# Kernel tuning notes

Hardware: AMD Instinct MI355X
Metric: run time of the kernel (lower is better)

## Reference

```python
import jax, jax.numpy as jnp
import numpy as np

CUTOFF = 5.0
N_PER_L = (20, 18, 16, 14)   # radial features per angular channel l (max_radial=20, Laplacian-eigenstate style taper)
M_PER_L = (1, 3, 5, 7)       # 2l+1
N_ATOMS = 10000
N_EDGES = 200000
N_SPECIES = 100
PSEUDO = 4

_FREQS = np.concatenate([np.arange(1, nl + 1) for nl in N_PER_L]).astype(np.float32)  # [sum(N_PER_L)]


def _radial(r):
    # r: [P] -> [P, sum(N_PER_L)]. Sine (spherical Laplacian eigenstate style) basis with smooth cosine cutoff.
    rc = jnp.clip(r, 0.0, CUTOFF)
    fc = 0.5 * (jnp.cos(jnp.pi * rc / CUTOFF) + 1.0)            # [P]
    return jnp.sin(jnp.asarray(_FREQS) * (jnp.pi / CUTOFF) * r[:, None]) * fc[:, None]


def _angular(R, r):
    # real spherical harmonics up to l=3, [P, 16], ordered l-major (m = -l..l)
    u = R / (r[:, None] + 1e-12)
    x, y, z = u[:, 0], u[:, 1], u[:, 2]
    x2, y2, z2 = x * x, y * y, z * z
    cols = [
        jnp.full_like(x, 0.28209479177387814),
        0.4886025119029199 * y, 0.4886025119029199 * z, 0.4886025119029199 * x,
        1.0925484305920792 * x * y, 1.0925484305920792 * y * z,
        0.31539156525252005 * (3.0 * z2 - 1.0),
        1.0925484305920792 * x * z, 0.5462742152960396 * (x2 - y2),
        0.5900435899266435 * y * (3.0 * x2 - y2), 2.890611442640554 * x * y * z,
        0.4570457994644658 * y * (5.0 * z2 - 1.0), 0.3731763325901154 * z * (5.0 * z2 - 3.0),
        0.4570457994644658 * x * (5.0 * z2 - 1.0), 1.445305721320277 * z * (x2 - y2),
        0.5900435899266435 * x * (x2 - 3.0 * y2),
    ]
    return jnp.stack(cols, axis=-1)


def setup_inputs() -> dict:
    key = jax.random.key(0)
    k1, k2, k3, k4, k5 = jax.random.split(key, 5)
    return {
        "R_ij": jax.random.normal(k1, (N_EDGES, 3), dtype=jnp.float32) * 1.5,
        "i": jnp.sort(jax.random.randint(k2, (N_EDGES,), 0, N_ATOMS)),
        "j": jax.random.randint(k3, (N_EDGES,), 0, N_ATOMS),
        "species": jax.random.randint(k4, (N_ATOMS,), 0, N_SPECIES),
        "species_embed": jax.random.normal(k5, (N_SPECIES, PSEUDO), dtype=jnp.float32),
    }


def reference(R_ij, i, j, species, species_embed):
    r = jnp.sqrt(jnp.sum(R_ij * R_ij, axis=-1))          # [P]
    radial = _radial(r)                                   # [P, sum n_l]
    angular = _angular(R_ij, r)                           # [P, 16]
    sp = species_embed[species[j]]                        # alchemical species channels, [P, 4]
    outs = []
    off_n = 0
    off_m = 0
    for nl, ml in zip(N_PER_L, M_PER_L):
        rl = radial[:, off_n:off_n + nl]                  # [P, n_l]
        al = angular[:, off_m:off_m + ml]                 # [P, 2l+1]
        e = jnp.einsum('pn,pm,pc->pmnc', rl, al, sp)      # fused outer product per edge
        outs.append(jax.ops.segment_sum(e, i, num_segments=N_ATOMS))  # [n_atoms, 2l+1, n_l, 4]
        off_n += nl
        off_m += ml
    return tuple(outs)
```

## Files before the change

kernel.cpp:

```cpp
#include <hip/hip_runtime.h>

#define N_ATOMS 10000
#define N_EDGES 200000
#define EB 64
#define FEAT 40
#define PI_F 3.14159265358979323846f
#define W_F  0.6283185307179586f

__global__ __launch_bounds__(256) void seg_starts_kernel(
    const int* __restrict__ seg_i, int* __restrict__ starts)
{
    const int a = blockIdx.x * blockDim.x + threadIdx.x;
    if (a > N_ATOMS) return;
    int lo = 0, hi = N_EDGES;
    while (lo < hi) {
        int mid = (lo + hi) >> 1;
        if (seg_i[mid] < a) lo = mid + 1; else hi = mid;
    }
    starts[a] = lo;
}

__global__ __launch_bounds__(128) void sph_expand_kernel(
    const float* __restrict__ R,
    const int*   __restrict__ starts,
    const int*   __restrict__ idx_j,
    const int*   __restrict__ species,
    const float* __restrict__ emb,
    float*       __restrict__ out)
{
    __shared__ float feat[EB][FEAT];
    const int atom = blockIdx.x;
    const int tid  = threadIdx.x;

    int m, np_, nl, offm; long base; int stride;
    {
        int t = tid;
        if (t < 10)      { m = 0;                 np_ = t;          nl = 20; offm = 0; base = 0;        stride = 80;  }
        else if (t < 37) { int q = t - 10; m = q / 9; np_ = q - 9*m; nl = 18; offm = 1; base = 800000;  stride = 216; }
        else if (t < 77) { int q = t - 37; m = q / 8; np_ = q - 8*m; nl = 16; offm = 4; base = 2960000; stride = 320; }
        else             { int q = t - 77; m = q / 7; np_ = q - 7*m; nl = 14; offm = 9; base = 6160000; stride = 392; }
    }
    const int n0   = 2 * np_;
    const int aidx = 20 + offm + m;
    const bool active = (tid < 126);

    float a0x=0.f, a0y=0.f, a0z=0.f, a0w=0.f;
    float a1x=0.f, a1y=0.f, a1z=0.f, a1w=0.f;

    const int start = starts[atom];
    const int end   = starts[atom + 1];

    for (int e0 = start; e0 < end; e0 += EB) {
        const int cnt = min(EB, end - e0);
        __syncthreads();
        if (tid < cnt) {
            const int g = e0 + tid;
            const int jj = idx_j[g];
            const float x = R[3*g + 0];
            const float y = R[3*g + 1];
            const float z = R[3*g + 2];
            const int sidx = species[jj];
            const float r   = sqrtf(x*x + y*y + z*z);
            const float inv = 1.0f / (r + 1e-12f);
            const float ux = x*inv, uy = y*inv, uz = z*inv;
            const float4 spv = *(const float4*)&emb[4 * sidx];

            const float t1 = W_F * r;
            const float s1 = sinf(t1);
            const float c1 = cosf(t1);
            const float fc = (r < 5.0f) ? (0.5f * (c1 + 1.0f)) : 0.0f;
            const float c2x = 2.0f * c1;

            float rb[20];
            {
                float sk_2 = 0.0f, sk_1 = s1;
                rb[0] = s1 * fc;
                #pragma unroll
                for (int k = 1; k < 20; ++k) {
                    const float sk = c2x * sk_1 - sk_2;
                    rb[k] = sk * fc;
                    sk_2 = sk_1; sk_1 = sk;
                }
            }

            const float x2 = ux*ux, y2 = uy*uy, z2 = uz*uz;
            const float c1a = 0.4886025119029199f;
            const float c2a = 1.0925484305920792f;
            float an[16];
            an[0]  = 0.28209479177387814f;
            an[1]  = c1a * uy;
            an[2]  = c1a * uz;
            an[3]  = c1a * ux;
            an[4]  = c2a * ux * uy;
            an[5]  = c2a * uy * uz;
            an[6]  = 0.31539156525252005f * (3.0f*z2 - 1.0f);
            an[7]  = c2a * ux * uz;
            an[8]  = 0.5462742152960396f * (x2 - y2);
            an[9]  = 0.5900435899266435f * uy * (3.0f*x2 - y2);
            an[10] = 2.890611442640554f  * ux * uy * uz;
            an[11] = 0.4570457994644658f * uy * (5.0f*z2 - 1.0f);
            an[12] = 0.3731763325901154f * uz * (5.0f*z2 - 3.0f);
            an[13] = 0.4570457994644658f * ux * (5.0f*z2 - 1.0f);
            an[14] = 1.445305721320277f  * uz * (x2 - y2);
            an[15] = 0.5900435899266435f * ux * (x2 - 3.0f*y2);

            float4* row = (float4*)&feat[tid][0];
            row[0] = float4{rb[0],  rb[1],  rb[2],  rb[3]};
            row[1] = float4{rb[4],  rb[5],  rb[6],  rb[7]};
            row[2] = float4{rb[8],  rb[9],  rb[10], rb[11]};
            row[3] = float4{rb[12], rb[13], rb[14], rb[15]};
            row[4] = float4{rb[16], rb[17], rb[18], rb[19]};
            row[5] = float4{an[0],  an[1],  an[2],  an[3]};
            row[6] = float4{an[4],  an[5],  an[6],  an[7]};
            row[7] = float4{an[8],  an[9],  an[10], an[11]};
            row[8] = float4{an[12], an[13], an[14], an[15]};
            row[9] = spv;
        }
        __syncthreads();
        if (active) {
            for (int s = 0; s < cnt; ++s) {
                const float* f = &feat[s][0];
                const float2 rv  = *(const float2*)(f + n0);
                const float  av  = f[aidx];
                const float4 spv = *(const float4*)(f + 36);
                const float p0 = rv.x * av;
                const float p1 = rv.y * av;
                a0x += p0 * spv.x; a0y += p0 * spv.y; a0z += p0 * spv.z; a0w += p0 * spv.w;
                a1x += p1 * spv.x; a1y += p1 * spv.y; a1z += p1 * spv.z; a1w += p1 * spv.w;
            }
        }
    }

    if (active) {
        const size_t o = (size_t)base + (size_t)atom * (size_t)stride + (size_t)(m * nl + n0) * 4;
        *(float4*)&out[o]     = float4{a0x, a0y, a0z, a0w};
        *(float4*)&out[o + 4] = float4{a1x, a1y, a1z, a1w};
    }
}

extern "C" void kernel_launch(void* const* d_in, const int* in_sizes, int n_in,
                              void* d_out, int out_size, void* d_ws, size_t ws_size,
                              hipStream_t stream) {
    const float* R    = (const float*)d_in[0];
    const int*   i_   = (const int*)  d_in[1];
    const int*   j_   = (const int*)  d_in[2];
    const int*   sp   = (const int*)  d_in[3];
    const float* emb  = (const float*)d_in[4];
    float* out = (float*)d_out;
    int*   starts = (int*)d_ws;

    seg_starts_kernel<<<(N_ATOMS + 256) / 256, 256, 0, stream>>>(i_, starts);
    sph_expand_kernel<<<N_ATOMS, 128, 0, stream>>>(R, starts, j_, sp, emb, out);
}
```

Before: 92.31 us.

## Register-block 4 radial x 2 angular outputs per thread, shrink block to one wavefront

```diff
diff --git a/kernel.cpp b/kernel.cpp
--- a/kernel.cpp
+++ b/kernel.cpp
@@ -2,8 +2,8 @@
 
 #define N_ATOMS 10000
 #define N_EDGES 200000
-#define EB 64
-#define FEAT 40
+#define EB   32
+#define ROWF 44
 #define PI_F 3.14159265358979323846f
 #define W_F  0.6283185307179586f
 
@@ -20,7 +20,35 @@
     starts[a] = lo;
 }
 
-__global__ __launch_bounds__(128) void sph_expand_kernel(
+#define TE(n0,aidx,w,m1,nl4,str,off) \
+  {(unsigned)((n0)|((aidx)<<5)|((w)<<11)|((m1)<<14)|((nl4)<<15)|((unsigned)(str)<<22)), (unsigned)(off)}
+__device__ const uint2 TBL[43] = {
+    TE( 0,20,4,0,80, 80,      0), TE( 4,20,4,0,80, 80,     16),
+    TE( 8,20,4,0,80, 80,     32), TE(12,20,4,0,80, 80,     48),
+    TE(16,20,4,0,80, 80,     64),
+    TE( 0,22,4,1,72,216, 800000), TE( 4,22,4,1,72,216, 800016),
+    TE( 8,22,4,1,72,216, 800032), TE(12,22,4,1,72,216, 800048),
+    TE(16,22,2,1,72,216, 800064),
+    TE( 0,24,4,0,72,216, 800144), TE( 4,24,4,0,72,216, 800160),
+    TE( 8,24,4,0,72,216, 800176), TE(12,24,4,0,72,216, 800192),
+    TE(16,24,2,0,72,216, 800208),
+    TE( 0,26,4,1,64,320,2960000), TE( 4,26,4,1,64,320,2960016),
+    TE( 8,26,4,1,64,320,2960032), TE(12,26,4,1,64,320,2960048),
+    TE( 0,28,4,1,64,320,2960128), TE( 4,28,4,1,64,320,2960144),
+    TE( 8,28,4,1,64,320,2960160), TE(12,28,4,1,64,320,2960176),
+    TE( 0,30,4,0,64,320,2960256), TE( 4,30,4,0,64,320,2960272),
+    TE( 8,30,4,0,64,320,2960288), TE(12,30,4,0,64,320,2960304),
+    TE( 0,32,4,1,56,392,6160000), TE( 4,32,4,1,56,392,6160016),
+    TE( 8,32,4,1,56,392,6160032), TE(12,32,2,1,56,392,6160048),
+    TE( 0,34,4,1,56,392,6160112), TE( 4,34,4,1,56,392,6160128),
+    TE( 8,34,4,1,56,392,6160144), TE(12,34,2,1,56,392,6160160),
+    TE( 0,36,4,1,56,392,6160224), TE( 4,36,4,1,56,392,6160240),
+    TE( 8,36,4,1,56,392,6160256), TE(12,36,2,1,56,392,6160272),
+    TE( 0,38,4,0,56,392,6160336), TE( 4,38,4,0,56,392,6160352),
+    TE( 8,38,4,0,56,392,6160368), TE(12,38,2,0,56,392,6160384),
+};
+
+__global__ __launch_bounds__(64) void sph_expand_kernel(
     const float* __restrict__ R,
     const int*   __restrict__ starts,
     const int*   __restrict__ idx_j,
@@ -28,24 +56,21 @@
     const float* __restrict__ emb,
     float*       __restrict__ out)
 {
-    __shared__ float feat[EB][FEAT];
+    __shared__ float feat[EB * ROWF];
     const int atom = blockIdx.x;
     const int tid  = threadIdx.x;
 
-    int m, np_, nl, offm; long base; int stride;
-    {
-        int t = tid;
-        if (t < 10)      { m = 0;                 np_ = t;          nl = 20; offm = 0; base = 0;        stride = 80;  }
-        else if (t < 37) { int q = t - 10; m = q / 9; np_ = q - 9*m; nl = 18; offm = 1; base = 800000;  stride = 216; }
-        else if (t < 77) { int q = t - 37; m = q / 8; np_ = q - 8*m; nl = 16; offm = 4; base = 2960000; stride = 320; }
-        else             { int q = t - 77; m = q / 7; np_ = q - 7*m; nl = 14; offm = 9; base = 6160000; stride = 392; }
-    }
-    const int n0   = 2 * np_;
-    const int aidx = 20 + offm + m;
-    const bool active = (tid < 126);
+    const uint2 tb = TBL[tid < 43 ? tid : 42];
+    const int n0     = tb.x & 31;
+    const int aidx   = (tb.x >> 5)  & 63;
+    const int w      = (tb.x >> 11) & 7;
+    const int m1     = (tb.x >> 14) & 1;
+    const int nl4    = (tb.x >> 15) & 127;
+    const int stride = (int)(tb.x >> 22);
+    const bool active = (tid < 43);
 
-    float a0x=0.f, a0y=0.f, a0z=0.f, a0w=0.f;
-    float a1x=0.f, a1y=0.f, a1z=0.f, a1w=0.f;
+    float4 a00{0,0,0,0}, a01{0,0,0,0}, a02{0,0,0,0}, a03{0,0,0,0};
+    float4 a10{0,0,0,0}, a11{0,0,0,0}, a12{0,0,0,0}, a13{0,0,0,0};
 
     const int start = starts[atom];
     const int end   = starts[atom + 1];
@@ -54,7 +79,7 @@
         const int cnt = min(EB, end - e0);
         __syncthreads();
         if (tid < cnt) {
-            const int g = e0 + tid;
+            const int g  = e0 + tid;
             const int jj = idx_j[g];
             const float x = R[3*g + 0];
             const float y = R[3*g + 1];
@@ -104,37 +129,49 @@
             an[14] = 1.445305721320277f  * uz * (x2 - y2);
             an[15] = 0.5900435899266435f * ux * (x2 - 3.0f*y2);
 
-            float4* row = (float4*)&feat[tid][0];
-            row[0] = float4{rb[0],  rb[1],  rb[2],  rb[3]};
-            row[1] = float4{rb[4],  rb[5],  rb[6],  rb[7]};
-            row[2] = float4{rb[8],  rb[9],  rb[10], rb[11]};
-            row[3] = float4{rb[12], rb[13], rb[14], rb[15]};
-            row[4] = float4{rb[16], rb[17], rb[18], rb[19]};
-            row[5] = float4{an[0],  an[1],  an[2],  an[3]};
-            row[6] = float4{an[4],  an[5],  an[6],  an[7]};
-            row[7] = float4{an[8],  an[9],  an[10], an[11]};
-            row[8] = float4{an[12], an[13], an[14], an[15]};
-            row[9] = spv;
+            float4* row = (float4*)&feat[tid * ROWF];
+            row[0]  = float4{rb[0],  rb[1],  rb[2],  rb[3]};
+            row[1]  = float4{rb[4],  rb[5],  rb[6],  rb[7]};
+            row[2]  = float4{rb[8],  rb[9],  rb[10], rb[11]};
+            row[3]  = float4{rb[12], rb[13], rb[14], rb[15]};
+            row[4]  = float4{rb[16], rb[17], rb[18], rb[19]};
+            row[5]  = float4{an[0],  0.0f,   an[1],  an[2]};
+            row[6]  = float4{an[3],  0.0f,   an[4],  an[5]};
+            row[7]  = float4{an[6],  an[7],  an[8],  0.0f};
+            row[8]  = float4{an[9],  an[10], an[11], an[12]};
+            row[9]  = float4{an[13], an[14], an[15], 0.0f};
+            row[10] = spv;
         }
         __syncthreads();
-        if (active) {
-            for (int s = 0; s < cnt; ++s) {
-                const float* f = &feat[s][0];
-                const float2 rv  = *(const float2*)(f + n0);
-                const float  av  = f[aidx];
-                const float4 spv = *(const float4*)(f + 36);
-                const float p0 = rv.x * av;
-                const float p1 = rv.y * av;
-                a0x += p0 * spv.x; a0y += p0 * spv.y; a0z += p0 * spv.z; a0w += p0 * spv.w;
-                a1x += p1 * spv.x; a1y += p1 * spv.y; a1z += p1 * spv.z; a1w += p1 * spv.w;
-            }
+
+        const float* f = feat;
+        for (int s = 0; s < cnt; ++s, f += ROWF) {
+            const float4 rv = *(const float4*)(f + n0);
+            const float2 av = *(const float2*)(f + aidx);
+            const float4 sv = *(const float4*)(f + 40);
+            float q;
+            q = rv.x*av.x; a00.x += q*sv.x; a00.y += q*sv.y; a00.z += q*sv.z; a00.w += q*sv.w;
+            q = rv.y*av.x; a01.x += q*sv.x; a01.y += q*sv.y; a01.z += q*sv.z; a01.w += q*sv.w;
+            q = rv.z*av.x; a02.x += q*sv.x; a02.y += q*sv.y; a02.z += q*sv.z; a02.w += q*sv.w;
+            q = rv.w*av.x; a03.x += q*sv.x; a03.y += q*sv.y; a03.z += q*sv.z; a03.w += q*sv.w;
+            q = rv.x*av.y; a10.x += q*sv.x; a10.y += q*sv.y; a10.z += q*sv.z; a10.w += q*sv.w;
+            q = rv.y*av.y; a11.x += q*sv.x; a11.y += q*sv.y; a11.z += q*sv.z; a11.w += q*sv.w;
+            q = rv.z*av.y; a12.x += q*sv.x; a12.y += q*sv.y; a12.z += q*sv.z; a12.w += q*sv.w;
+            q = rv.w*av.y; a13.x += q*sv.x; a13.y += q*sv.y; a13.z += q*sv.z; a13.w += q*sv.w;
         }
     }
 
     if (active) {
-        const size_t o = (size_t)base + (size_t)atom * (size_t)stride + (size_t)(m * nl + n0) * 4;
-        *(float4*)&out[o]     = float4{a0x, a0y, a0z, a0w};
-        *(float4*)&out[o + 4] = float4{a1x, a1y, a1z, a1w};
+        float* o = out + (size_t)tb.y + (size_t)atom * (size_t)stride;
+        *(float4*)(o + 0) = a00;
+        *(float4*)(o + 4) = a01;
+        if (w == 4) { *(float4*)(o + 8) = a02; *(float4*)(o + 12) = a03; }
+        if (m1) {
+            float* o1 = o + nl4;
+            *(float4*)(o1 + 0) = a10;
+            *(float4*)(o1 + 4) = a11;
+            if (w == 4) { *(float4*)(o1 + 8) = a12; *(float4*)(o1 + 12) = a13; }
+        }
     }
 }
 
@@ -150,5 +187,5 @@
     int*   starts = (int*)d_ws;
 
     seg_starts_kernel<<<(N_ATOMS + 256) / 256, 256, 0, stream>>>(i_, starts);
-    sph_expand_kernel<<<N_ATOMS, 128, 0, stream>>>(R, starts, j_, sp, emb, out);
+    sph_expand_kernel<<<N_ATOMS, 64, 0, stream>>>(R, starts, j_, sp, emb, out);
 }
```

Result: slower. 97.24 us (+5.3%).
